# Kernel tuning notes

Hardware: AMD Instinct MI355X
Metric: run time of the kernel (lower is better)

Reference implementation:

```python
import jax, jax.numpy as jnp
import numpy as np

B, N1, N2, D = 8, 2048, 2048, 512

def setup_inputs() -> dict:
    key = jax.random.key(0)
    k1, k2, k3, k4 = jax.random.split(key, 4)
    input1 = jax.random.normal(k1, (B, N1, D), dtype=jnp.float32)
    input2 = jax.random.normal(k2, (B, N2, D), dtype=jnp.float32)
    # nn.Linear(D, D): weight [D, D] (out, in), bias [D]
    W_w = jax.random.normal(k3, (D, D), dtype=jnp.float32) * (1.0 / np.sqrt(D))
    W_b = jax.random.normal(k4, (D,), dtype=jnp.float32) * 0.01
    return {"input1": input1, "input2": input2, "W_w": W_w, "W_b": W_b}

def reference(input1, input2, W_w, W_b):
    # q = W(input1): [B, N1, D]
    q = jnp.einsum('bnd,od->bno', input1, W_w) + W_b
    # unscaled scores softmax over last dim (keys N2)
    attn = jax.nn.softmax(jnp.einsum('bnd,bmd->bnm', q, input2), axis=-1)  # [B, N1, N2]
    output1 = jnp.einsum('bnm,bmd->bnd', attn, input2)   # [B, N1, D]
    output2 = jnp.einsum('bnm,bnd->bmd', attn, input1)   # attn^T @ input1 -> [B, N2, D]
    return (output1, output2)
```

## Files before the change

### kernel.cpp

```cpp
#include <hip/hip_runtime.h>


typedef _Float16 f16x8 __attribute__((ext_vector_type(8)));
typedef _Float16 f16x4 __attribute__((ext_vector_type(4)));
typedef float floatx4 __attribute__((ext_vector_type(4)));
typedef __attribute__((address_space(1))) const void* gptr_t;
typedef __attribute__((address_space(3))) void* lptr_t;

union F8 { f16x8 v; _Float16 h[8]; unsigned short u[8]; unsigned w[4]; };
union F4 { f16x4 v; _Float16 h[4]; unsigned u2[2]; };

__device__ __forceinline__ void gld16(const void* g, void* l) {
    __builtin_amdgcn_global_load_lds((gptr_t)g, (lptr_t)l, 16, 0, 0);
}
__device__ __forceinline__ floatx4 mfma16(f16x8 a, f16x8 b, floatx4 c) {
    return __builtin_amdgcn_mfma_f32_16x16x32_f16(a, b, c, 0, 0, 0);
}

template <int ROWS>
__device__ __forceinline__ void stage64(const _Float16* g, int ldg,
                                        _Float16* lds, int tid) {
#pragma unroll
    for (int c = 0; c < (ROWS * 8) / 256; ++c) {
        const int q = c * 256 + tid;
        const int row = q >> 3;
        const int oct = (q & 7) ^ (row & 7);
        gld16(g + (size_t)row * ldg + oct * 8, lds + q * 8);
    }
}
__device__ __forceinline__ f16x8 ldfrag64(const _Float16* lds, int row, int j) {
    return *(const f16x8*)&lds[row * 64 + ((j ^ (row & 7)) << 3)];
}
__device__ __forceinline__ f16x8 ldfragA(const _Float16* lds, int row, int j) {
    return *(const f16x8*)&lds[row * 64 + ((j ^ ((row >> 1) & 7)) << 3)];
}

#define TS 66
__global__ __launch_bounds__(256) void k_prep2(
    const float* __restrict__ in1, const float* __restrict__ in2,
    _Float16* __restrict__ x16, _Float16* __restrict__ xt,
    _Float16* __restrict__ k16, _Float16* __restrict__ vt)
{
    __shared__ __align__(16) _Float16 T[64 * TS];
    const int z = blockIdx.z;
    const int b = z & 7;
    const float* src = (z < 8 ? in1 : in2);
    _Float16* rowo = (z < 8 ? x16 : k16);
    _Float16* colo = (z < 8 ? xt : vt);
    const int d0 = blockIdx.x * 64, n0 = blockIdx.y * 64;
    const float* Sp = src + (size_t)b * 2048 * 512;
    _Float16* Rp = rowo + (size_t)b * 2048 * 512;
    _Float16* Cp = colo + (size_t)b * 512 * 2048;
    const int t = threadIdx.x;

#pragma unroll
    for (int c = 0; c < 4; c++) {
        const int q = c * 256 + t, r = q >> 4, c4 = q & 15;
        const float4 g = *(const float4*)(Sp + (size_t)(n0 + r) * 512 + d0 + c4 * 4);
        F4 w;
        w.h[0] = (_Float16)g.x; w.h[1] = (_Float16)g.y;
        w.h[2] = (_Float16)g.z; w.h[3] = (_Float16)g.w;
        *(f16x4*)(Rp + (size_t)(n0 + r) * 512 + d0 + c4 * 4) = w.v;
        *(unsigned*)&T[r * TS + c4 * 4]     = w.u2[0];
        *(unsigned*)&T[r * TS + c4 * 4 + 2] = w.u2[1];
    }
    __syncthreads();
    const int c8 = t & 7, drp = (t >> 3) * 2;
    F8 w0, w1;
#pragma unroll
    for (int i = 0; i < 8; i++) {
        const unsigned g = *(const unsigned*)&T[(c8 * 8 + i) * TS + drp];
        w0.u[i] = (unsigned short)(g & 0xffffu);
        w1.u[i] = (unsigned short)(g >> 16);
    }
    *(f16x8*)(Cp + (size_t)(d0 + drp) * 2048 + n0 + c8 * 8) = w0.v;
    *(f16x8*)(Cp + (size_t)(d0 + drp + 1) * 2048 + n0 + c8 * 8) = w1.v;
}

__global__ __launch_bounds__(256) void k_cvt(const float* __restrict__ src,
                                             _Float16* __restrict__ dst)
{
    const size_t i = ((size_t)blockIdx.x * 256 + threadIdx.x) * 8;
    float4 a = *(const float4*)(src + i);
    float4 b = *(const float4*)(src + i + 4);
    F8 w;
    w.h[0] = (_Float16)a.x; w.h[1] = (_Float16)a.y;
    w.h[2] = (_Float16)a.z; w.h[3] = (_Float16)a.w;
    w.h[4] = (_Float16)b.x; w.h[5] = (_Float16)b.y;
    w.h[6] = (_Float16)b.z; w.h[7] = (_Float16)b.w;
    *(f16x8*)(dst + i) = w.v;
}

__global__ __launch_bounds__(256, 4) void k_qgemm16(
    const _Float16* __restrict__ A, const _Float16* __restrict__ W,
    const float* __restrict__ bias, _Float16* __restrict__ q)
{
    __shared__ __align__(16) _Float16 As[128 * 64], Bs[128 * 64];
    const int tid = threadIdx.x;
    const int lane = tid & 63, wave = tid >> 6;
    const int wM = (wave >> 1) * 64, wN = (wave & 1) * 64;
    const int lrow = lane & 15, kq = lane >> 4;
    const int bi = blockIdx.x;
    const int r0 = (bi >> 2) * 128, c0 = (bi & 3) * 128;

    floatx4 acc[4][4];
#pragma unroll
    for (int i = 0; i < 4; i++)
#pragma unroll
        for (int j = 0; j < 4; j++) acc[i][j] = (floatx4){0.f, 0.f, 0.f, 0.f};

    for (int k0 = 0; k0 < 512; k0 += 64) {
        stage64<128>(A + (size_t)r0 * 512 + k0, 512, As, tid);
        stage64<128>(W + (size_t)c0 * 512 + k0, 512, Bs, tid);
        __syncthreads();
#pragma unroll
        for (int ks = 0; ks < 2; ks++) {
            f16x8 a[4], b[4];
#pragma unroll
            for (int i = 0; i < 4; i++) {
                a[i] = ldfrag64(As, wM + i * 16 + lrow, ks * 4 + kq);
                b[i] = ldfrag64(Bs, wN + i * 16 + lrow, ks * 4 + kq);
            }
#pragma unroll
            for (int mi = 0; mi < 4; mi++)
#pragma unroll
                for (int ni = 0; ni < 4; ni++)
                    acc[mi][ni] = mfma16(a[mi], b[ni], acc[mi][ni]);
        }
        __syncthreads();
    }
#pragma unroll
    for (int ni = 0; ni < 4; ni++) {
        const int col = c0 + wN + ni * 16 + lrow;
        const float bv = bias[col];
#pragma unroll
        for (int mi = 0; mi < 4; mi++) {
            const int row = r0 + wM + mi * 16 + kq * 4;
#pragma unroll
            for (int r = 0; r < 4; r++)
                q[(size_t)(row + r) * 512 + col] = (_Float16)(acc[mi][ni][r] + bv);
        }
    }
}

__global__ __launch_bounds__(256, 4) void k_scores16(
    const _Float16* __restrict__ q, const _Float16* __restrict__ k,
    _Float16* __restrict__ S)
{
    __shared__ __align__(16) _Float16 As[128 * 64], Bs[128 * 64];
    const int tid = threadIdx.x;
    const int lane = tid & 63, wave = tid >> 6;
    const int wM = (wave >> 1) * 64, wN = (wave & 1) * 64;
    const int lrow = lane & 15, kq = lane >> 4;
    const int bi = blockIdx.x;
    const int bz = bi & 7, t = bi >> 3;
    const int c0 = (t & 15) * 128, r0 = (t >> 4) * 128;
    const _Float16* qp = q + (size_t)bz * 2048 * 512;
    const _Float16* kp = k + (size_t)bz * 2048 * 512;
    _Float16* Sp = S + (size_t)bz * 2048 * 2048;

    floatx4 acc[4][4];
#pragma unroll
    for (int i = 0; i < 4; i++)
#pragma unroll
        for (int j = 0; j < 4; j++) acc[i][j] = (floatx4){0.f, 0.f, 0.f, 0.f};

    for (int k0 = 0; k0 < 512; k0 += 64) {
        stage64<128>(qp + (size_t)r0 * 512 + k0, 512, As, tid);
        stage64<128>(kp + (size_t)c0 * 512 + k0, 512, Bs, tid);
        __syncthreads();
#pragma unroll
        for (int ks = 0; ks < 2; ks++) {
            f16x8 a[4], b[4];
#pragma unroll
            for (int i = 0; i < 4; i++) {
                a[i] = ldfrag64(As, wM + i * 16 + lrow, ks * 4 + kq);
                b[i] = ldfrag64(Bs, wN + i * 16 + lrow, ks * 4 + kq);
            }
#pragma unroll
            for (int mi = 0; mi < 4; mi++)
#pragma unroll
                for (int ni = 0; ni < 4; ni++)
                    acc[mi][ni] = mfma16(a[mi], b[ni], acc[mi][ni]);
        }
        __syncthreads();
    }
#pragma unroll
    for (int mi = 0; mi < 4; mi++)
#pragma unroll
        for (int ni = 0; ni < 4; ni++) {
            const int row = r0 + wM + mi * 16 + kq * 4;
            const int col = c0 + wN + ni * 16 + lrow;
            _Float16* dst = Sp + (size_t)row * 2048 + col;
#pragma unroll
            for (int r = 0; r < 4; r++) dst[(size_t)r * 2048] = (_Float16)acc[mi][ni][r];
        }
}

__global__ __launch_bounds__(256) void k_softmax(const _Float16* __restrict__ S,
                                                 _Float16* __restrict__ P)
{
    const int wave = threadIdx.x >> 6, lane = threadIdx.x & 63;
    const int row = blockIdx.x * 4 + wave;
    const _Float16* s = S + (size_t)row * 2048;
    _Float16* p = P + (size_t)row * 2048;

    F8 raw[4];
    float v[32];
#pragma unroll
    for (int c = 0; c < 4; c++) {
        raw[c].v = *(const f16x8*)(s + c * 512 + lane * 8);
#pragma unroll
        for (int i = 0; i < 8; i++) v[c * 8 + i] = (float)raw[c].h[i];
    }
    float m = v[0];
#pragma unroll
    for (int i = 1; i < 32; i++) m = fmaxf(m, v[i]);
#pragma unroll
    for (int off = 32; off >= 1; off >>= 1) m = fmaxf(m, __shfl_xor(m, off));

    float sum = 0.f;
#pragma unroll
    for (int i = 0; i < 32; i++) { v[i] = __expf(v[i] - m); sum += v[i]; }
#pragma unroll
    for (int off = 32; off >= 1; off >>= 1) sum += __shfl_xor(sum, off);
    const float inv = 1.0f / sum;

#pragma unroll
    for (int c = 0; c < 4; c++) {
        F8 w;
#pragma unroll
        for (int i = 0; i < 8; i++) w.h[i] = (_Float16)(v[c * 8 + i] * inv);
        *(f16x8*)(p + c * 512 + lane * 8) = w.v;
    }
}

__device__ __forceinline__ void loadtr16(const _Float16* Pp, int r0, int mPair,
                                         int kBase, int k0, unsigned (&u)[16]) {
#pragma unroll
    for (int j = 0; j < 16; j++)
        u[j] = *(const unsigned*)(
            Pp + (size_t)(k0 + kBase + j) * 2048 + r0 + mPair);
}

__global__ __launch_bounds__(256, 2) void k_out12(
    const _Float16* __restrict__ P, const _Float16* __restrict__ Vt,
    const _Float16* __restrict__ Xt, float* __restrict__ O1,
    float* __restrict__ O2)
{
    __shared__ __align__(16) _Float16 lds[32768];
    const int tid = threadIdx.x;
    const int lane = tid & 63, wave = tid >> 6;
    const int wM = (wave >> 1) * 64, wN = (wave & 1) * 64;
    const int lrow = lane & 15, kq = lane >> 4;
    const bool isO2 = blockIdx.x & 1;
    const int bi = blockIdx.x >> 1;
    const int bz = bi & 7, t = bi >> 3;
    const int c0 = (t & 3) * 128, r0 = (t >> 2) * 128;
    const _Float16* Pp = P + (size_t)bz * 2048 * 2048;
    const _Float16* Bp = (isO2 ? Xt : Vt) + (size_t)bz * 512 * 2048;
    float* Op = (isO2 ? O2 : O1) + (size_t)bz * 2048 * 512;

    floatx4 acc[4][4];
#pragma unroll
    for (int i = 0; i < 4; i++)
#pragma unroll
        for (int j = 0; j < 4; j++) acc[i][j] = (floatx4){0.f, 0.f, 0.f, 0.f};

    if (!isO2) {
        stage64<128>(Pp + (size_t)r0 * 2048, 2048, lds, tid);
        stage64<128>(Bp + (size_t)c0 * 2048, 2048, lds + 16384, tid);
        int cur = 0;
        for (int k0 = 0; k0 < 2048; k0 += 64) {
            if (k0 < 2048 - 64) {
                stage64<128>(Pp + (size_t)r0 * 2048 + k0 + 64, 2048,
                             lds + (cur ^ 1) * 8192, tid);
                stage64<128>(Bp + (size_t)c0 * 2048 + k0 + 64, 2048,
                             lds + 16384 + (cur ^ 1) * 8192, tid);
                asm volatile("s_waitcnt vmcnt(8)" ::: "memory");
            } else {
                asm volatile("s_waitcnt vmcnt(0)" ::: "memory");
            }
            __builtin_amdgcn_s_barrier();
            const _Float16* Ac = lds + cur * 8192;
            const _Float16* Bc = lds + 16384 + cur * 8192;
#pragma unroll
            for (int ks = 0; ks < 2; ks++) {
                f16x8 a[4], b[4];
#pragma unroll
                for (int i = 0; i < 4; i++) {
                    a[i] = ldfrag64(Ac, wM + i * 16 + lrow, ks * 4 + kq);
                    b[i] = ldfrag64(Bc, wN + i * 16 + lrow, ks * 4 + kq);
                }
#pragma unroll
                for (int mi = 0; mi < 4; mi++)
#pragma unroll
                    for (int ni = 0; ni < 4; ni++)
                        acc[mi][ni] = mfma16(a[mi], b[ni], acc[mi][ni]);
            }
            __builtin_amdgcn_s_barrier();
            cur ^= 1;
        }
    } else {
        _Float16* As_ = lds;
        const int mPair = (tid & 63) * 2;
        const int kBase = (tid >> 6) * 16;

        unsigned u[16];
        loadtr16(Pp, r0, mPair, kBase, 0, u);
        stage64<128>(Bp + (size_t)c0 * 2048, 2048, lds + 8192, tid);
        int cur = 0;
        for (int k0 = 0; k0 < 2048; k0 += 64) {
            const int sw = (mPair >> 1) & 7;
#pragma unroll
            for (int half = 0; half < 2; half++) {
                const int oct = (kBase >> 3) + half;
                F8 w0, w1;
#pragma unroll
                for (int j = 0; j < 8; j++) {
                    const unsigned g = u[half * 8 + j];
                    w0.u[j] = (unsigned short)(g & 0xffffu);
                    w1.u[j] = (unsigned short)(g >> 16);
                }
                *(f16x8*)&As_[mPair * 64 + ((oct ^ sw) << 3)] = w0.v;
                *(f16x8*)&As_[(mPair + 1) * 64 + ((oct ^ sw) << 3)] = w1.v;
            }
            if (k0 < 2048 - 64) {
                loadtr16(Pp, r0, mPair, kBase, k0 + 64, u);
                stage64<128>(Bp + (size_t)c0 * 2048 + k0 + 64, 2048,
                             lds + 8192 + (cur ^ 1) * 8192, tid);
                asm volatile("s_waitcnt vmcnt(20) lgkmcnt(0)" ::: "memory");
            } else {
                asm volatile("s_waitcnt vmcnt(0) lgkmcnt(0)" ::: "memory");
            }
            __builtin_amdgcn_s_barrier();
            const _Float16* Bc = lds + 8192 + cur * 8192;
#pragma unroll
            for (int ks = 0; ks < 2; ks++) {
                f16x8 a[4], b[4];
#pragma unroll
                for (int i = 0; i < 4; i++) {
                    a[i] = ldfragA(As_, wM + i * 16 + lrow, ks * 4 + kq);
                    b[i] = ldfrag64(Bc, wN + i * 16 + lrow, ks * 4 + kq);
                }
#pragma unroll
                for (int mi = 0; mi < 4; mi++)
#pragma unroll
                    for (int ni = 0; ni < 4; ni++)
                        acc[mi][ni] = mfma16(a[mi], b[ni], acc[mi][ni]);
            }
            __builtin_amdgcn_s_barrier();
            cur ^= 1;
        }
    }
#pragma unroll
    for (int mi = 0; mi < 4; mi++)
#pragma unroll
        for (int ni = 0; ni < 4; ni++) {
            const int row = r0 + wM + mi * 16 + kq * 4;
            const int col = c0 + wN + ni * 16 + lrow;
            float* dst = Op + (size_t)row * 512 + col;
#pragma unroll
            for (int r = 0; r < 4; r++) dst[(size_t)r * 512] = acc[mi][ni][r];
        }
}

extern "C" void kernel_launch(void* const* d_in, const int* in_sizes, int n_in,
                              void* d_out, int out_size, void* d_ws, size_t ws_size,
                              hipStream_t stream)
{
    (void)in_sizes; (void)n_in; (void)out_size; (void)ws_size;
    const float* in1 = (const float*)d_in[0];
    const float* in2 = (const float*)d_in[1];
    const float* Ww  = (const float*)d_in[2];
    const float* Wb  = (const float*)d_in[3];
    float* out = (float*)d_out;

    char* ws = (char*)d_ws;
    _Float16* S   = (_Float16*)ws;
    _Float16* P   = (_Float16*)(ws + 67108864ull);
    _Float16* q16 = (_Float16*)(ws + 134217728ull);
    _Float16* x16 = (_Float16*)(ws + 150994944ull);
    _Float16* k16 = (_Float16*)(ws + 167772160ull);
    _Float16* vt  = (_Float16*)(ws + 184549376ull);
    _Float16* xt  = (_Float16*)(ws + 201326592ull);
    _Float16* w16 = (_Float16*)(ws + 218103808ull);

    k_prep2<<<dim3(8, 32, 16), 256, 0, stream>>>(in1, in2, x16, xt, k16, vt);
    k_cvt <<<128, 256, 0, stream>>>(Ww, w16);
    k_qgemm16<<<512, 256, 0, stream>>>(x16, w16, Wb, q16);
    k_scores16<<<2048, 256, 0, stream>>>(q16, k16, S);
    k_softmax<<<4096, 256, 0, stream>>>(S, P);
    k_out12<<<1024, 256, 0, stream>>>(P, vt, xt, out, out + 8388608);
}
```

Measured before the change: 272.9 us.

## Double-buffer LDS staging in GEMMs and remap blocks for XCD-aware locality

The q-projection and scores GEMMs now use double-buffered LDS. The next K-tile is issued with global_load_lds while the current tile feeds the MFMAs, synchronised with explicit vmcnt waits and barriers. All three GEMM kernels also remap blockIdx so that blocks sharing a batch or row panel land on the same XCD (blockIdx & 7 selects the group), which is meant to improve L2 reuse. Occupancy drops from 4 to 2 blocks per CU because LDS use doubles.

Result: slower. 278.8 us (+2.2%).

```diff
diff --git a/kernel.cpp b/kernel.cpp
--- a/kernel.cpp
+++ b/kernel.cpp
@@ -91,172 +91,199 @@
     *(f16x8*)(dst + i) = w.v;
 }
 
-__global__ __launch_bounds__(256, 4) void k_qgemm16(
+__global__ __launch_bounds__(256, 2) void k_qgemm16(
     const _Float16* __restrict__ A, const _Float16* __restrict__ W,
     const float* __restrict__ bias, _Float16* __restrict__ q)
-{
-    __shared__ __align__(16) _Float16 As[128 * 64], Bs[128 * 64];
-    const int tid = threadIdx.x;
-    const int lane = tid & 63, wave = tid >> 6;
-    const int wM = (wave >> 1) * 64, wN = (wave & 1) * 64;
-    const int lrow = lane & 15, kq = lane >> 4;
-    const int bi = blockIdx.x;
-    const int r0 = (bi >> 2) * 128, c0 = (bi & 3) * 128;
-
-    floatx4 acc[4][4];
-#pragma unroll
-    for (int i = 0; i < 4; i++)
-#pragma unroll
-        for (int j = 0; j < 4; j++) acc[i][j] = (floatx4){0.f, 0.f, 0.f, 0.f};
-
-    for (int k0 = 0; k0 < 512; k0 += 64) {
-        stage64<128>(A + (size_t)r0 * 512 + k0, 512, As, tid);
-        stage64<128>(W + (size_t)c0 * 512 + k0, 512, Bs, tid);
-        __syncthreads();
-#pragma unroll
-        for (int ks = 0; ks < 2; ks++) {
-            f16x8 a[4], b[4];
-#pragma unroll
-            for (int i = 0; i < 4; i++) {
-                a[i] = ldfrag64(As, wM + i * 16 + lrow, ks * 4 + kq);
-                b[i] = ldfrag64(Bs, wN + i * 16 + lrow, ks * 4 + kq);
-            }
-#pragma unroll
-            for (int mi = 0; mi < 4; mi++)
-#pragma unroll
-                for (int ni = 0; ni < 4; ni++)
-                    acc[mi][ni] = mfma16(a[mi], b[ni], acc[mi][ni]);
-        }
-        __syncthreads();
-    }
-#pragma unroll
-    for (int ni = 0; ni < 4; ni++) {
-        const int col = c0 + wN + ni * 16 + lrow;
-        const float bv = bias[col];
-#pragma unroll
-        for (int mi = 0; mi < 4; mi++) {
-            const int row = r0 + wM + mi * 16 + kq * 4;
-#pragma unroll
-            for (int r = 0; r < 4; r++)
-                q[(size_t)(row + r) * 512 + col] = (_Float16)(acc[mi][ni][r] + bv);
-        }
-    }
-}
-
-__global__ __launch_bounds__(256, 4) void k_scores16(
-    const _Float16* __restrict__ q, const _Float16* __restrict__ k,
-    _Float16* __restrict__ S)
-{
-    __shared__ __align__(16) _Float16 As[128 * 64], Bs[128 * 64];
-    const int tid = threadIdx.x;
-    const int lane = tid & 63, wave = tid >> 6;
-    const int wM = (wave >> 1) * 64, wN = (wave & 1) * 64;
-    const int lrow = lane & 15, kq = lane >> 4;
-    const int bi = blockIdx.x;
-    const int bz = bi & 7, t = bi >> 3;
-    const int c0 = (t & 15) * 128, r0 = (t >> 4) * 128;
-    const _Float16* qp = q + (size_t)bz * 2048 * 512;
-    const _Float16* kp = k + (size_t)bz * 2048 * 512;
-    _Float16* Sp = S + (size_t)bz * 2048 * 2048;
-
-    floatx4 acc[4][4];
-#pragma unroll
-    for (int i = 0; i < 4; i++)
-#pragma unroll
-        for (int j = 0; j < 4; j++) acc[i][j] = (floatx4){0.f, 0.f, 0.f, 0.f};
-
-    for (int k0 = 0; k0 < 512; k0 += 64) {
-        stage64<128>(qp + (size_t)r0 * 512 + k0, 512, As, tid);
-        stage64<128>(kp + (size_t)c0 * 512 + k0, 512, Bs, tid);
-        __syncthreads();
-#pragma unroll
-        for (int ks = 0; ks < 2; ks++) {
-            f16x8 a[4], b[4];
-#pragma unroll
-            for (int i = 0; i < 4; i++) {
-                a[i] = ldfrag64(As, wM + i * 16 + lrow, ks * 4 + kq);
-                b[i] = ldfrag64(Bs, wN + i * 16 + lrow, ks * 4 + kq);
-            }
-#pragma unroll
-            for (int mi = 0; mi < 4; mi++)
-#pragma unroll
-                for (int ni = 0; ni < 4; ni++)
-                    acc[mi][ni] = mfma16(a[mi], b[ni], acc[mi][ni]);
-        }
-        __syncthreads();
-    }
-#pragma unroll
-    for (int mi = 0; mi < 4; mi++)
-#pragma unroll
-        for (int ni = 0; ni < 4; ni++) {
-            const int row = r0 + wM + mi * 16 + kq * 4;
-            const int col = c0 + wN + ni * 16 + lrow;
-            _Float16* dst = Sp + (size_t)row * 2048 + col;
-#pragma unroll
-            for (int r = 0; r < 4; r++) dst[(size_t)r * 2048] = (_Float16)acc[mi][ni][r];
-        }
-}
-
-__global__ __launch_bounds__(256) void k_softmax(const _Float16* __restrict__ S,
-                                                 _Float16* __restrict__ P)
-{
-    const int wave = threadIdx.x >> 6, lane = threadIdx.x & 63;
-    const int row = blockIdx.x * 4 + wave;
-    const _Float16* s = S + (size_t)row * 2048;
-    _Float16* p = P + (size_t)row * 2048;
-
-    F8 raw[4];
-    float v[32];
-#pragma unroll
-    for (int c = 0; c < 4; c++) {
-        raw[c].v = *(const f16x8*)(s + c * 512 + lane * 8);
-#pragma unroll
-        for (int i = 0; i < 8; i++) v[c * 8 + i] = (float)raw[c].h[i];
-    }
-    float m = v[0];
-#pragma unroll
-    for (int i = 1; i < 32; i++) m = fmaxf(m, v[i]);
-#pragma unroll
-    for (int off = 32; off >= 1; off >>= 1) m = fmaxf(m, __shfl_xor(m, off));
-
-    float sum = 0.f;
-#pragma unroll
-    for (int i = 0; i < 32; i++) { v[i] = __expf(v[i] - m); sum += v[i]; }
-#pragma unroll
-    for (int off = 32; off >= 1; off >>= 1) sum += __shfl_xor(sum, off);
-    const float inv = 1.0f / sum;
-
-#pragma unroll
-    for (int c = 0; c < 4; c++) {
-        F8 w;
-#pragma unroll
-        for (int i = 0; i < 8; i++) w.h[i] = (_Float16)(v[c * 8 + i] * inv);
-        *(f16x8*)(p + c * 512 + lane * 8) = w.v;
-    }
-}
-
-__device__ __forceinline__ void loadtr16(const _Float16* Pp, int r0, int mPair,
-                                         int kBase, int k0, unsigned (&u)[16]) {
-#pragma unroll
-    for (int j = 0; j < 16; j++)
-        u[j] = *(const unsigned*)(
-            Pp + (size_t)(k0 + kBase + j) * 2048 + r0 + mPair);
-}
-
-__global__ __launch_bounds__(256, 2) void k_out12(
-    const _Float16* __restrict__ P, const _Float16* __restrict__ Vt,
-    const _Float16* __restrict__ Xt, float* __restrict__ O1,
-    float* __restrict__ O2)
 {
     __shared__ __align__(16) _Float16 lds[32768];
     const int tid = threadIdx.x;
     const int lane = tid & 63, wave = tid >> 6;
     const int wM = (wave >> 1) * 64, wN = (wave & 1) * 64;
     const int lrow = lane & 15, kq = lane >> 4;
-    const bool isO2 = blockIdx.x & 1;
-    const int bi = blockIdx.x >> 1;
-    const int bz = bi & 7, t = bi >> 3;
-    const int c0 = (t & 3) * 128, r0 = (t >> 2) * 128;
+    const int remap = (blockIdx.x & 7) * 64 + (blockIdx.x >> 3);
+    const int r0 = (remap >> 2) * 128, c0 = (remap & 3) * 128;
+
+    floatx4 acc[4][4];
+#pragma unroll
+    for (int i = 0; i < 4; i++)
+#pragma unroll
+        for (int j = 0; j < 4; j++) acc[i][j] = (floatx4){0.f, 0.f, 0.f, 0.f};
+
+    stage64<128>(A + (size_t)r0 * 512, 512, lds, tid);
+    stage64<128>(W + (size_t)c0 * 512, 512, lds + 16384, tid);
+    int cur = 0;
+    for (int k0 = 0; k0 < 512; k0 += 64) {
+        if (k0 < 512 - 64) {
+            stage64<128>(A + (size_t)r0 * 512 + k0 + 64, 512,
+                         lds + (cur ^ 1) * 8192, tid);
+            stage64<128>(W + (size_t)c0 * 512 + k0 + 64, 512,
+                         lds + 16384 + (cur ^ 1) * 8192, tid);
+            asm volatile("s_waitcnt vmcnt(8)" ::: "memory");
+        } else {
+            asm volatile("s_waitcnt vmcnt(0)" ::: "memory");
+        }
+        __builtin_amdgcn_s_barrier();
+        const _Float16* Ac = lds + cur * 8192;
+        const _Float16* Bc = lds + 16384 + cur * 8192;
+#pragma unroll
+        for (int ks = 0; ks < 2; ks++) {
+            f16x8 a[4], b[4];
+#pragma unroll
+            for (int i = 0; i < 4; i++) {
+                a[i] = ldfrag64(Ac, wM + i * 16 + lrow, ks * 4 + kq);
+                b[i] = ldfrag64(Bc, wN + i * 16 + lrow, ks * 4 + kq);
+            }
+#pragma unroll
+            for (int mi = 0; mi < 4; mi++)
+#pragma unroll
+                for (int ni = 0; ni < 4; ni++)
+                    acc[mi][ni] = mfma16(a[mi], b[ni], acc[mi][ni]);
+        }
+        __builtin_amdgcn_s_barrier();
+        cur ^= 1;
+    }
+#pragma unroll
+    for (int ni = 0; ni < 4; ni++) {
+        const int col = c0 + wN + ni * 16 + lrow;
+        const float bv = bias[col];
+#pragma unroll
+        for (int mi = 0; mi < 4; mi++) {
+            const int row = r0 + wM + mi * 16 + kq * 4;
+#pragma unroll
+            for (int r = 0; r < 4; r++)
+                q[(size_t)(row + r) * 512 + col] = (_Float16)(acc[mi][ni][r] + bv);
+        }
+    }
+}
+
+__global__ __launch_bounds__(256, 2) void k_scores16(
+    const _Float16* __restrict__ q, const _Float16* __restrict__ k,
+    _Float16* __restrict__ S)
+{
+    __shared__ __align__(16) _Float16 lds[32768];
+    const int tid = threadIdx.x;
+    const int lane = tid & 63, wave = tid >> 6;
+    const int wM = (wave >> 1) * 64, wN = (wave & 1) * 64;
+    const int lrow = lane & 15, kq = lane >> 4;
+    const int remap = (blockIdx.x & 7) * 256 + (blockIdx.x >> 3);
+    const int bz = remap >> 8;
+    const int c0 = ((remap >> 4) & 15) * 128, r0 = (remap & 15) * 128;
+    const _Float16* qp = q + (size_t)bz * 2048 * 512;
+    const _Float16* kp = k + (size_t)bz * 2048 * 512;
+    _Float16* Sp = S + (size_t)bz * 2048 * 2048;
+
+    floatx4 acc[4][4];
+#pragma unroll
+    for (int i = 0; i < 4; i++)
+#pragma unroll
+        for (int j = 0; j < 4; j++) acc[i][j] = (floatx4){0.f, 0.f, 0.f, 0.f};
+
+    stage64<128>(qp + (size_t)r0 * 512, 512, lds, tid);
+    stage64<128>(kp + (size_t)c0 * 512, 512, lds + 16384, tid);
+    int cur = 0;
+    for (int k0 = 0; k0 < 512; k0 += 64) {
+        if (k0 < 512 - 64) {
+            stage64<128>(qp + (size_t)r0 * 512 + k0 + 64, 512,
+                         lds + (cur ^ 1) * 8192, tid);
+            stage64<128>(kp + (size_t)c0 * 512 + k0 + 64, 512,
+                         lds + 16384 + (cur ^ 1) * 8192, tid);
+            asm volatile("s_waitcnt vmcnt(8)" ::: "memory");
+        } else {
+            asm volatile("s_waitcnt vmcnt(0)" ::: "memory");
+        }
+        __builtin_amdgcn_s_barrier();
+        const _Float16* Ac = lds + cur * 8192;
+        const _Float16* Bc = lds + 16384 + cur * 8192;
+#pragma unroll
+        for (int ks = 0; ks < 2; ks++) {
+            f16x8 a[4], b[4];
+#pragma unroll
+            for (int i = 0; i < 4; i++) {
+                a[i] = ldfrag64(Ac, wM + i * 16 + lrow, ks * 4 + kq);
+                b[i] = ldfrag64(Bc, wN + i * 16 + lrow, ks * 4 + kq);
+            }
+#pragma unroll
+            for (int mi = 0; mi < 4; mi++)
+#pragma unroll
+                for (int ni = 0; ni < 4; ni++)
+                    acc[mi][ni] = mfma16(a[mi], b[ni], acc[mi][ni]);
+        }
+        __builtin_amdgcn_s_barrier();
+        cur ^= 1;
+    }
+#pragma unroll
+    for (int mi = 0; mi < 4; mi++)
+#pragma unroll
+        for (int ni = 0; ni < 4; ni++) {
+            const int row = r0 + wM + mi * 16 + kq * 4;
+            const int col = c0 + wN + ni * 16 + lrow;
+            _Float16* dst = Sp + (size_t)row * 2048 + col;
+#pragma unroll
+            for (int r = 0; r < 4; r++) dst[(size_t)r * 2048] = (_Float16)acc[mi][ni][r];
+        }
+}
+
+__global__ __launch_bounds__(256) void k_softmax(const _Float16* __restrict__ S,
+                                                 _Float16* __restrict__ P)
+{
+    const int wave = threadIdx.x >> 6, lane = threadIdx.x & 63;
+    const int row = blockIdx.x * 4 + wave;
+    const _Float16* s = S + (size_t)row * 2048;
+    _Float16* p = P + (size_t)row * 2048;
+
+    F8 raw[4];
+    float v[32];
+#pragma unroll
+    for (int c = 0; c < 4; c++) {
+        raw[c].v = *(const f16x8*)(s + c * 512 + lane * 8);
+#pragma unroll
+        for (int i = 0; i < 8; i++) v[c * 8 + i] = (float)raw[c].h[i];
+    }
+    float m = v[0];
+#pragma unroll
+    for (int i = 1; i < 32; i++) m = fmaxf(m, v[i]);
+#pragma unroll
+    for (int off = 32; off >= 1; off >>= 1) m = fmaxf(m, __shfl_xor(m, off));
+
+    float sum = 0.f;
+#pragma unroll
+    for (int i = 0; i < 32; i++) { v[i] = __expf(v[i] - m); sum += v[i]; }
+#pragma unroll
+    for (int off = 32; off >= 1; off >>= 1) sum += __shfl_xor(sum, off);
+    const float inv = 1.0f / sum;
+
+#pragma unroll
+    for (int c = 0; c < 4; c++) {
+        F8 w;
+#pragma unroll
+        for (int i = 0; i < 8; i++) w.h[i] = (_Float16)(v[c * 8 + i] * inv);
+        *(f16x8*)(p + c * 512 + lane * 8) = w.v;
+    }
+}
+
+__device__ __forceinline__ void loadtr16(const _Float16* Pp, int r0, int mPair,
+                                         int kBase, int k0, unsigned (&u)[16]) {
+#pragma unroll
+    for (int j = 0; j < 16; j++)
+        u[j] = *(const unsigned*)(
+            Pp + (size_t)(k0 + kBase + j) * 2048 + r0 + mPair);
+}
+
+__global__ __launch_bounds__(256, 2) void k_out12(
+    const _Float16* __restrict__ P, const _Float16* __restrict__ Vt,
+    const _Float16* __restrict__ Xt, float* __restrict__ O1,
+    float* __restrict__ O2)
+{
+    __shared__ __align__(16) _Float16 lds[32768];
+    const int tid = threadIdx.x;
+    const int lane = tid & 63, wave = tid >> 6;
+    const int wM = (wave >> 1) * 64, wN = (wave & 1) * 64;
+    const int lrow = lane & 15, kq = lane >> 4;
+    const int remap = (blockIdx.x & 7) * 128 + (blockIdx.x >> 3);
+    const int bz = remap >> 7;
+    const int rest = remap & 127;
+    const bool isO2 = rest & 1;
+    const int c0 = ((rest >> 5) & 3) * 128, r0 = ((rest >> 1) & 15) * 128;
     const _Float16* Pp = P + (size_t)bz * 2048 * 2048;
     const _Float16* Bp = (isO2 ? Xt : Vt) + (size_t)bz * 512 * 2048;
     float* Op = (isO2 ? O2 : O1) + (size_t)bz * 2048 * 512;
```

## Drop LDS double buffering in output GEMM to raise occupancy to four blocks

Applied to the files above, without the earlier changes.

Removes the double-buffered LDS pipeline in the P@V / P^T@X kernel, halving shared memory to 32KB and raising the launch-bounds occupancy hint from 2 to 4 blocks per CU. Each k-step now stages its tile and synchronizes before computing, so loads no longer overlap MFMA within a block. The intent is to hide latency through more resident waves instead, at the risk of exposed load latency and tighter register limits (spills with 64 accumulator floats per thread).

Result: no change. 272.7 us (-0.1%).

```diff
diff --git a/kernel.cpp b/kernel.cpp
--- a/kernel.cpp
+++ b/kernel.cpp
@@ -243,12 +243,12 @@
             Pp + (size_t)(k0 + kBase + j) * 2048 + r0 + mPair);
 }
 
-__global__ __launch_bounds__(256, 2) void k_out12(
+__global__ __launch_bounds__(256, 4) void k_out12(
     const _Float16* __restrict__ P, const _Float16* __restrict__ Vt,
     const _Float16* __restrict__ Xt, float* __restrict__ O1,
     float* __restrict__ O2)
 {
-    __shared__ __align__(16) _Float16 lds[32768];
+    __shared__ __align__(16) _Float16 lds[16384];
     const int tid = threadIdx.x;
     const int lane = tid & 63, wave = tid >> 6;
     const int wM = (wave >> 1) * 64, wN = (wave & 1) * 64;
@@ -268,29 +268,17 @@
         for (int j = 0; j < 4; j++) acc[i][j] = (floatx4){0.f, 0.f, 0.f, 0.f};
 
     if (!isO2) {
-        stage64<128>(Pp + (size_t)r0 * 2048, 2048, lds, tid);
-        stage64<128>(Bp + (size_t)c0 * 2048, 2048, lds + 16384, tid);
-        int cur = 0;
         for (int k0 = 0; k0 < 2048; k0 += 64) {
-            if (k0 < 2048 - 64) {
-                stage64<128>(Pp + (size_t)r0 * 2048 + k0 + 64, 2048,
-                             lds + (cur ^ 1) * 8192, tid);
-                stage64<128>(Bp + (size_t)c0 * 2048 + k0 + 64, 2048,
-                             lds + 16384 + (cur ^ 1) * 8192, tid);
-                asm volatile("s_waitcnt vmcnt(8)" ::: "memory");
-            } else {
-                asm volatile("s_waitcnt vmcnt(0)" ::: "memory");
-            }
-            __builtin_amdgcn_s_barrier();
-            const _Float16* Ac = lds + cur * 8192;
-            const _Float16* Bc = lds + 16384 + cur * 8192;
+            stage64<128>(Pp + (size_t)r0 * 2048 + k0, 2048, lds, tid);
+            stage64<128>(Bp + (size_t)c0 * 2048 + k0, 2048, lds + 8192, tid);
+            __syncthreads();
 #pragma unroll
             for (int ks = 0; ks < 2; ks++) {
                 f16x8 a[4], b[4];
 #pragma unroll
                 for (int i = 0; i < 4; i++) {
-                    a[i] = ldfrag64(Ac, wM + i * 16 + lrow, ks * 4 + kq);
-                    b[i] = ldfrag64(Bc, wN + i * 16 + lrow, ks * 4 + kq);
+                    a[i] = ldfrag64(lds, wM + i * 16 + lrow, ks * 4 + kq);
+                    b[i] = ldfrag64(lds + 8192, wN + i * 16 + lrow, ks * 4 + kq);
                 }
 #pragma unroll
                 for (int mi = 0; mi < 4; mi++)
@@ -298,8 +286,7 @@
                     for (int ni = 0; ni < 4; ni++)
                         acc[mi][ni] = mfma16(a[mi], b[ni], acc[mi][ni]);
             }
-            __builtin_amdgcn_s_barrier();
-            cur ^= 1;
+            __syncthreads();
         }
     } else {
         _Float16* As_ = lds;
@@ -308,8 +295,6 @@
 
         unsigned u[16];
         loadtr16(Pp, r0, mPair, kBase, 0, u);
-        stage64<128>(Bp + (size_t)c0 * 2048, 2048, lds + 8192, tid);
-        int cur = 0;
         for (int k0 = 0; k0 < 2048; k0 += 64) {
             const int sw = (mPair >> 1) & 7;
 #pragma unroll
@@ -325,23 +310,17 @@
                 *(f16x8*)&As_[mPair * 64 + ((oct ^ sw) << 3)] = w0.v;
                 *(f16x8*)&As_[(mPair + 1) * 64 + ((oct ^ sw) << 3)] = w1.v;
             }
-            if (k0 < 2048 - 64) {
+            stage64<128>(Bp + (size_t)c0 * 2048 + k0, 2048, lds + 8192, tid);
+            __syncthreads();
+            if (k0 < 2048 - 64)
                 loadtr16(Pp, r0, mPair, kBase, k0 + 64, u);
-                stage64<128>(Bp + (size_t)c0 * 2048 + k0 + 64, 2048,
-                             lds + 8192 + (cur ^ 1) * 8192, tid);
-                asm volatile("s_waitcnt vmcnt(20) lgkmcnt(0)" ::: "memory");
-            } else {
-                asm volatile("s_waitcnt vmcnt(0) lgkmcnt(0)" ::: "memory");
-            }
-            __builtin_amdgcn_s_barrier();
-            const _Float16* Bc = lds + 8192 + cur * 8192;
 #pragma unroll
             for (int ks = 0; ks < 2; ks++) {
                 f16x8 a[4], b[4];
 #pragma unroll
                 for (int i = 0; i < 4; i++) {
                     a[i] = ldfragA(As_, wM + i * 16 + lrow, ks * 4 + kq);
-                    b[i] = ldfrag64(Bc, wN + i * 16 + lrow, ks * 4 + kq);
+                    b[i] = ldfrag64(lds + 8192, wN + i * 16 + lrow, ks * 4 + kq);
                 }
 #pragma unroll
                 for (int mi = 0; mi < 4; mi++)
@@ -349,8 +328,7 @@
                     for (int ni = 0; ni < 4; ni++)
                         acc[mi][ni] = mfma16(a[mi], b[ni], acc[mi][ni]);
             }
-            __builtin_amdgcn_s_barrier();
-            cur ^= 1;
+            __syncthreads();
         }
     }
 #pragma unroll
```
